# Performance work log

Measured on AMD Instinct MI355X. Metric: run time of the kernel, lower is better.

The kernel has to match this reference:

```python
import jax, jax.numpy as jnp
import numpy as np

FP8_MAX = 448.0  # float8_e4m3fn max


def setup_inputs() -> dict:
    key = jax.random.key(0)
    k1, k2, k3 = jax.random.split(key, 3)
    B, S, Hq, Hkv, D = 64, 4096, 32, 8, 128
    q = jax.random.normal(k1, (B, Hq, D), jnp.float32)
    k_cache = jax.random.normal(k2, (B, S, Hkv, D), jnp.float32)
    v_cache = jax.random.normal(k3, (B, S, Hkv, D), jnp.float32)
    quant_scale = jnp.ones((1,), jnp.float32)  # static per-tensor FP8 scale
    return {"q": q, "k_cache": k_cache, "v_cache": v_cache, "quant_scale": quant_scale}


def reference(q, k_cache, v_cache, quant_scale):
    # Decode attention (1 query token per request) with GQA, then static
    # per-tensor FP8 quantization of the attention output.
    B, Hq, D = q.shape
    Hkv = k_cache.shape[2]
    G = Hq // Hkv  # query heads per kv head
    sm_scale = 1.0 / np.sqrt(D).astype(np.float32)

    qg = q.reshape(B, Hkv, G, D)
    # scores: [B, Hkv, G, S]
    scores = jnp.einsum('bhgd,bshd->bhgs', qg, k_cache) * sm_scale
    p = jax.nn.softmax(scores, axis=-1)
    # out: [B, Hkv, G, D] -> [B, Hq*D]
    o = jnp.einsum('bhgs,bshd->bhgd', p, v_cache).reshape(B, Hq * D)

    # Static per-tensor FP8 quant: clamp(x / scale) -> fp8, returned as the
    # fp8-representable values in fp32 for comparison.
    x = o / quant_scale[0]
    y = jnp.clip(x, -FP8_MAX, FP8_MAX).astype(jnp.float8_e4m3fn).astype(jnp.float32)
    return y
```

## Files before the change

kernel.cpp:

```cpp
#include <hip/hip_runtime.h>
#include <math.h>

#define NB    64
#define NS    4096
#define NHQ   32
#define NHKV  8
#define ND    128
#define NG    4
#define WAVES 8
#define NTHREADS (WAVES*64)

__device__ __forceinline__ float quant_e4m3(float x) {
    float a = fabsf(x);
    a = fminf(a, 448.0f);
    unsigned ui = __float_as_uint(a);
    int e  = (int)(ui >> 23) - 127;
    int se = (e < -6 ? -6 : e) - 3;
    float stp = __uint_as_float((unsigned)(se + 127) << 23);
    float qv  = rintf(a / stp) * stp;
    return copysignf(qv, x);
}

__global__ __launch_bounds__(NTHREADS, 4) void attn_decode_quant(
    const float* __restrict__ qin,
    const float* __restrict__ kc,
    const float* __restrict__ vc,
    const float* __restrict__ qscale,
    float* __restrict__ out)
{
    __shared__ double s_acc[WAVES][NG][ND];
    __shared__ double s_l[WAVES][NG];
    __shared__ float  s_m[WAVES][NG];
    __shared__ double s_w[WAVES][NG];
    __shared__ double s_lt[NG];

    const int bh   = blockIdx.x;
    const int b    = bh >> 3;
    const int h    = bh & 7;
    const int tid  = threadIdx.x;
    const int wave = tid >> 6;
    const int lane = tid & 63;
    const int half = lane >> 5;
    const int l32  = lane & 31;

    const float sm_scale = (float)(1.0 / (double)sqrtf(128.0f));

    float4 qf[NG];
    {
        const float* qb = qin + ((size_t)b * NHQ + (size_t)h * NG) * ND + l32 * 4;
        #pragma unroll
        for (int g = 0; g < NG; ++g) qf[g] = *(const float4*)(qb + g * ND);
    }

    const size_t rs = (size_t)NHKV * ND;
    const float* kb = kc + ((size_t)b * NS * NHKV + h) * ND;
    const float* vb = vc + ((size_t)b * NS * NHKV + h) * ND;

    const int s0  = wave * (NS / WAVES) + half;
    const int NIT = (NS / WAVES) / 2;

    const float* kp = kb + (size_t)s0 * rs + l32 * 4;
    const float* vp = vb + (size_t)s0 * rs + l32 * 4;

    float  m[NG];
    double l[NG];
    double acc[NG][4];
    #pragma unroll
    for (int g = 0; g < NG; ++g) {
        m[g] = -INFINITY; l[g] = 0.0;
        #pragma unroll
        for (int j = 0; j < 4; ++j) acc[g][j] = 0.0;
    }

    float4 ka  = *(const float4*)(kp);
    float4 va  = *(const float4*)(vp);
    float4 kn  = *(const float4*)(kp + 2 * rs);
    float4 vn  = *(const float4*)(vp + 2 * rs);

    for (int i = 0; i < NIT; ++i) {
        float4 kf = ka, vf = va;
        ka = kn; va = vn;
        int ip = (i + 2 < NIT) ? (i + 2) : (NIT - 1);
        kn = *(const float4*)(kp + (size_t)ip * 2 * rs);
        vn = *(const float4*)(vp + (size_t)ip * 2 * rs);

        float sg[NG];
        #pragma unroll
        for (int g = 0; g < NG; ++g) {
            float s = qf[g].x * kf.x;
            s = fmaf(qf[g].y, kf.y, s);
            s = fmaf(qf[g].z, kf.z, s);
            s = fmaf(qf[g].w, kf.w, s);
            sg[g] = s;
        }
        #pragma unroll
        for (int g = 0; g < NG; ++g) {
            #pragma unroll
            for (int mask = 1; mask < 32; mask <<= 1)
                sg[g] += __shfl_xor(sg[g], mask);
        }

        double v0d = (double)vf.x, v1d = (double)vf.y;
        double v2d = (double)vf.z, v3d = (double)vf.w;

        #pragma unroll
        for (int g = 0; g < NG; ++g) {
            float s = sg[g] * sm_scale;
            float p;
            if (s > m[g]) {
                double corr = exp((double)(m[g] - s));
                l[g] *= corr;
                acc[g][0] *= corr; acc[g][1] *= corr;
                acc[g][2] *= corr; acc[g][3] *= corr;
                m[g] = s;
                p = 1.0f;
            } else {
                p = expf(s - m[g]);
            }
            double pd = (double)p;
            l[g] += pd;
            acc[g][0] = fma(pd, v0d, acc[g][0]);
            acc[g][1] = fma(pd, v1d, acc[g][1]);
            acc[g][2] = fma(pd, v2d, acc[g][2]);
            acc[g][3] = fma(pd, v3d, acc[g][3]);
        }
    }

    #pragma unroll
    for (int g = 0; g < NG; ++g) {
        float  mo = __shfl_xor(m[g], 32);
        double lo = __shfl_xor(l[g], 32);
        double a0 = __shfl_xor(acc[g][0], 32);
        double a1 = __shfl_xor(acc[g][1], 32);
        double a2 = __shfl_xor(acc[g][2], 32);
        double a3 = __shfl_xor(acc[g][3], 32);
        float M2 = fmaxf(m[g], mo);
        double w  = exp((double)(m[g] - M2));
        double wo = exp((double)(mo   - M2));
        acc[g][0] = acc[g][0] * w + a0 * wo;
        acc[g][1] = acc[g][1] * w + a1 * wo;
        acc[g][2] = acc[g][2] * w + a2 * wo;
        acc[g][3] = acc[g][3] * w + a3 * wo;
        l[g] = l[g] * w + lo * wo;
        m[g] = M2;
    }

    if (half == 0) {
        #pragma unroll
        for (int g = 0; g < NG; ++g) {
            #pragma unroll
            for (int j = 0; j < 4; ++j)
                s_acc[wave][g][l32 * 4 + j] = acc[g][j];
        }
        if (l32 == 0) {
            #pragma unroll
            for (int g = 0; g < NG; ++g) { s_m[wave][g] = m[g]; s_l[wave][g] = l[g]; }
        }
    }
    __syncthreads();

    if (tid < NG) {
        int g = tid;
        float M = -INFINITY;
        for (int pa = 0; pa < WAVES; ++pa) M = fmaxf(M, s_m[pa][g]);
        double ltot = 0.0;
        for (int pa = 0; pa < WAVES; ++pa) {
            double w = exp((double)(s_m[pa][g] - M));
            s_w[pa][g] = w;
            ltot += s_l[pa][g] * w;
        }
        s_lt[g] = ltot;
    }
    __syncthreads();

    {
        const float qs = qscale[0];
        int g = tid >> 7;
        int d = tid & 127;
        double o = 0.0;
        for (int pa = 0; pa < WAVES; ++pa)
            o += s_acc[pa][g][d] * s_w[pa][g];
        o /= s_lt[g];
        float x = (float)o;
        x = x / qs;
        out[((size_t)b * NHQ + (size_t)(h * NG + g)) * ND + d] = quant_e4m3(x);
    }
}

extern "C" void kernel_launch(void* const* d_in, const int* in_sizes, int n_in,
                              void* d_out, int out_size, void* d_ws, size_t ws_size,
                              hipStream_t stream) {
    (void)in_sizes; (void)n_in; (void)d_ws; (void)ws_size; (void)out_size;
    const float* q  = (const float*)d_in[0];
    const float* k  = (const float*)d_in[1];
    const float* v  = (const float*)d_in[2];
    const float* qs = (const float*)d_in[3];
    float* o = (float*)d_out;
    hipLaunchKernelGGL(attn_decode_quant, dim3(NB * NHKV), dim3(NTHREADS), 0, stream,
                       q, k, v, qs, o);
}
```

Measured before the change: 406.4 us.

## Process four keys per wave round with 16-lane dot products and LDS-shared probabilities

Restructures the decode loop so each wave handles four keys per round: 16-lane groups compute full 128-dim dot products, which halves shuffle depth and exp count per key. A wave-wide row max drives the online softmax, and probabilities are exchanged through LDS so each half-wave accumulates V for two keys. K and V are read with nontemporal loads. The change cuts per-key shuffle and exp overhead in a loop dominated by latency and ALU work. In exchange it adds LDS traffic and relies on implicit wave-level ordering of the LDS writes and reads with no barrier.

```diff
diff --git a/kernel.cpp b/kernel.cpp
--- a/kernel.cpp
+++ b/kernel.cpp
@@ -9,6 +9,9 @@
 #define NG    4
 #define WAVES 8
 #define NTHREADS (WAVES*64)
+#define ROUNDS ((NS/WAVES)/4)
+
+typedef float f32x4 __attribute__((ext_vector_type(4)));
 
 __device__ __forceinline__ float quant_e4m3(float x) {
     float a = fabsf(x);
@@ -19,6 +22,11 @@
     float stp = __uint_as_float((unsigned)(se + 127) << 23);
     float qv  = rintf(a / stp) * stp;
     return copysignf(qv, x);
+}
+
+__device__ __forceinline__ float4 ntld(const float* p) {
+    f32x4 r = __builtin_nontemporal_load((const f32x4*)p);
+    return make_float4(r.x, r.y, r.z, r.w);
 }
 
 __global__ __launch_bounds__(NTHREADS, 4) void attn_decode_quant(
@@ -33,6 +41,7 @@
     __shared__ float  s_m[WAVES][NG];
     __shared__ double s_w[WAVES][NG];
     __shared__ double s_lt[NG];
+    __shared__ float  p_lds[WAVES][16];
 
     const int bh   = blockIdx.x;
     const int b    = bh >> 3;
@@ -40,27 +49,32 @@
     const int tid  = threadIdx.x;
     const int wave = tid >> 6;
     const int lane = tid & 63;
+    const int c    = lane >> 4;
+    const int e    = lane & 15;
     const int half = lane >> 5;
     const int l32  = lane & 31;
 
     const float sm_scale = (float)(1.0 / (double)sqrtf(128.0f));
 
-    float4 qf[NG];
+    float4 qf[NG][2];
     {
-        const float* qb = qin + ((size_t)b * NHQ + (size_t)h * NG) * ND + l32 * 4;
-        #pragma unroll
-        for (int g = 0; g < NG; ++g) qf[g] = *(const float4*)(qb + g * ND);
+        const float* qb = qin + ((size_t)b * NHQ + (size_t)h * NG) * ND;
+        #pragma unroll
+        for (int g = 0; g < NG; ++g) {
+            #pragma unroll
+            for (int j = 0; j < 2; ++j)
+                qf[g][j] = *(const float4*)(qb + g * ND + 4 * e + 64 * j);
+        }
     }
 
     const size_t rs = (size_t)NHKV * ND;
     const float* kb = kc + ((size_t)b * NS * NHKV + h) * ND;
     const float* vb = vc + ((size_t)b * NS * NHKV + h) * ND;
 
-    const int s0  = wave * (NS / WAVES) + half;
-    const int NIT = (NS / WAVES) / 2;
-
-    const float* kp = kb + (size_t)s0 * rs + l32 * 4;
-    const float* vp = vb + (size_t)s0 * rs + l32 * 4;
+    const int wbase = wave * (NS / WAVES);
+
+    const float* kp = kb + (size_t)(wbase + c) * rs + 4 * e;
+    const float* vp = vb + (size_t)(wbase + half) * rs + 4 * l32;
 
     float  m[NG];
     double l[NG];
@@ -72,77 +86,106 @@
         for (int j = 0; j < 4; ++j) acc[g][j] = 0.0;
     }
 
-    float4 ka  = *(const float4*)(kp);
-    float4 va  = *(const float4*)(vp);
-    float4 kn  = *(const float4*)(kp + 2 * rs);
-    float4 vn  = *(const float4*)(vp + 2 * rs);
-
-    for (int i = 0; i < NIT; ++i) {
-        float4 kf = ka, vf = va;
-        ka = kn; va = vn;
-        int ip = (i + 2 < NIT) ? (i + 2) : (NIT - 1);
-        kn = *(const float4*)(kp + (size_t)ip * 2 * rs);
-        vn = *(const float4*)(vp + (size_t)ip * 2 * rs);
-
-        float sg[NG];
-        #pragma unroll
-        for (int g = 0; g < NG; ++g) {
-            float s = qf[g].x * kf.x;
-            s = fmaf(qf[g].y, kf.y, s);
-            s = fmaf(qf[g].z, kf.z, s);
-            s = fmaf(qf[g].w, kf.w, s);
-            sg[g] = s;
-        }
-        #pragma unroll
-        for (int g = 0; g < NG; ++g) {
-            #pragma unroll
-            for (int mask = 1; mask < 32; mask <<= 1)
-                sg[g] += __shfl_xor(sg[g], mask);
-        }
-
-        double v0d = (double)vf.x, v1d = (double)vf.y;
-        double v2d = (double)vf.z, v3d = (double)vf.w;
-
-        #pragma unroll
-        for (int g = 0; g < NG; ++g) {
-            float s = sg[g] * sm_scale;
-            float p;
-            if (s > m[g]) {
-                double corr = exp((double)(m[g] - s));
+    float4 kka = ntld(kp);
+    float4 kkb = ntld(kp + 64);
+
+    for (int r = 0; r < ROUNDS; ++r) {
+        const float* vr = vp + (size_t)(4 * r) * rs;
+        float4 va0 = ntld(vr);
+        float4 va1 = ntld(vr + 2 * rs);
+
+        int rn = (r + 1 < ROUNDS) ? (r + 1) : r;
+        const float* kn = kp + (size_t)(4 * rn) * rs;
+        float4 knA = ntld(kn);
+        float4 knB = ntld(kn + 64);
+
+        float s[NG];
+        #pragma unroll
+        for (int g = 0; g < NG; ++g) {
+            float sd = qf[g][0].x * kka.x;
+            sd = fmaf(qf[g][0].y, kka.y, sd);
+            sd = fmaf(qf[g][0].z, kka.z, sd);
+            sd = fmaf(qf[g][0].w, kka.w, sd);
+            sd = fmaf(qf[g][1].x, kkb.x, sd);
+            sd = fmaf(qf[g][1].y, kkb.y, sd);
+            sd = fmaf(qf[g][1].z, kkb.z, sd);
+            sd = fmaf(qf[g][1].w, kkb.w, sd);
+            s[g] = sd;
+        }
+        #pragma unroll
+        for (int g = 0; g < NG; ++g) {
+            #pragma unroll
+            for (int mask = 1; mask < 16; mask <<= 1)
+                s[g] += __shfl_xor(s[g], mask);
+            s[g] *= sm_scale;
+        }
+
+        float p[NG];
+        #pragma unroll
+        for (int g = 0; g < NG; ++g) {
+            float rm = s[g];
+            rm = fmaxf(rm, __shfl_xor(rm, 16));
+            rm = fmaxf(rm, __shfl_xor(rm, 32));
+            if (rm > m[g]) {
+                double corr = exp((double)(m[g] - rm));
                 l[g] *= corr;
                 acc[g][0] *= corr; acc[g][1] *= corr;
                 acc[g][2] *= corr; acc[g][3] *= corr;
-                m[g] = s;
-                p = 1.0f;
-            } else {
-                p = expf(s - m[g]);
+                m[g] = rm;
             }
-            double pd = (double)p;
-            l[g] += pd;
-            acc[g][0] = fma(pd, v0d, acc[g][0]);
-            acc[g][1] = fma(pd, v1d, acc[g][1]);
-            acc[g][2] = fma(pd, v2d, acc[g][2]);
-            acc[g][3] = fma(pd, v3d, acc[g][3]);
-        }
+            p[g] = expf(s[g] - m[g]);
+            l[g] += (double)p[g];
+        }
+
+        {
+            float pw = (e == 0) ? p[0] : (e == 1) ? p[1] : (e == 2) ? p[2] : p[3];
+            if (e < 4) p_lds[wave][c * 4 + e] = pw;
+        }
+
+        float4 pA = *(const float4*)&p_lds[wave][half * 4];
+        float4 pB = *(const float4*)&p_lds[wave][8 + half * 4];
+        {
+            double vx = (double)va0.x, vy = (double)va0.y;
+            double vz = (double)va0.z, vw = (double)va0.w;
+            double p0 = (double)pA.x, p1 = (double)pA.y;
+            double p2 = (double)pA.z, p3 = (double)pA.w;
+            acc[0][0] = fma(p0, vx, acc[0][0]); acc[0][1] = fma(p0, vy, acc[0][1]);
+            acc[0][2] = fma(p0, vz, acc[0][2]); acc[0][3] = fma(p0, vw, acc[0][3]);
+            acc[1][0] = fma(p1, vx, acc[1][0]); acc[1][1] = fma(p1, vy, acc[1][1]);
+            acc[1][2] = fma(p1, vz, acc[1][2]); acc[1][3] = fma(p1, vw, acc[1][3]);
+            acc[2][0] = fma(p2, vx, acc[2][0]); acc[2][1] = fma(p2, vy, acc[2][1]);
+            acc[2][2] = fma(p2, vz, acc[2][2]); acc[2][3] = fma(p2, vw, acc[2][3]);
+            acc[3][0] = fma(p3, vx, acc[3][0]); acc[3][1] = fma(p3, vy, acc[3][1]);
+            acc[3][2] = fma(p3, vz, acc[3][2]); acc[3][3] = fma(p3, vw, acc[3][3]);
+        }
+        {
+            double vx = (double)va1.x, vy = (double)va1.y;
+            double vz = (double)va1.z, vw = (double)va1.w;
+            double p0 = (double)pB.x, p1 = (double)pB.y;
+            double p2 = (double)pB.z, p3 = (double)pB.w;
+            acc[0][0] = fma(p0, vx, acc[0][0]); acc[0][1] = fma(p0, vy, acc[0][1]);
+            acc[0][2] = fma(p0, vz, acc[0][2]); acc[0][3] = fma(p0, vw, acc[0][3]);
+            acc[1][0] = fma(p1, vx, acc[1][0]); acc[1][1] = fma(p1, vy, acc[1][1]);
+            acc[1][2] = fma(p1, vz, acc[1][2]); acc[1][3] = fma(p1, vw, acc[1][3]);
+            acc[2][0] = fma(p2, vx, acc[2][0]); acc[2][1] = fma(p2, vy, acc[2][1]);
+            acc[2][2] = fma(p2, vz, acc[2][2]); acc[2][3] = fma(p2, vw, acc[2][3]);
+            acc[3][0] = fma(p3, vx, acc[3][0]); acc[3][1] = fma(p3, vy, acc[3][1]);
+            acc[3][2] = fma(p3, vz, acc[3][2]); acc[3][3] = fma(p3, vw, acc[3][3]);
+        }
+
+        kka = knA; kkb = knB;
     }
 
     #pragma unroll
     for (int g = 0; g < NG; ++g) {
-        float  mo = __shfl_xor(m[g], 32);
-        double lo = __shfl_xor(l[g], 32);
-        double a0 = __shfl_xor(acc[g][0], 32);
-        double a1 = __shfl_xor(acc[g][1], 32);
-        double a2 = __shfl_xor(acc[g][2], 32);
-        double a3 = __shfl_xor(acc[g][3], 32);
-        float M2 = fmaxf(m[g], mo);
-        double w  = exp((double)(m[g] - M2));
-        double wo = exp((double)(mo   - M2));
-        acc[g][0] = acc[g][0] * w + a0 * wo;
-        acc[g][1] = acc[g][1] * w + a1 * wo;
-        acc[g][2] = acc[g][2] * w + a2 * wo;
-        acc[g][3] = acc[g][3] * w + a3 * wo;
-        l[g] = l[g] * w + lo * wo;
-        m[g] = M2;
+        l[g] += __shfl_xor(l[g], 16);
+        l[g] += __shfl_xor(l[g], 32);
+    }
+    #pragma unroll
+    for (int g = 0; g < NG; ++g) {
+        #pragma unroll
+        for (int j = 0; j < 4; ++j)
+            acc[g][j] += __shfl_xor(acc[g][j], 32);
     }
 
     if (half == 0) {
```

Result: slower. 493.2 us (+21.4%).
